# Optimization experiments

Measured on AMD Instinct MI355X. Metric: run time of the kernel, lower is better.

## Reference

```python
import jax, jax.numpy as jnp
import numpy as np

B, N_IN, NV, F = 1, 65536, 1, 64
N_OUT, K = 16384, 16
N_DIST, N_PHI, OUT = 4, 8, 256
DIST_MAX = 0.1  # grid_layers[level_out].min_dist stand-in


def setup_inputs() -> dict:
    key = jax.random.key(0)
    ks = jax.random.split(key, 6)
    x = jax.random.normal(ks[0], (B, N_IN, NV, F), dtype=jnp.float32)
    nh_idx = jax.random.randint(ks[1], (N_OUT, K), 0, N_IN)  # neighbor gather indices
    d_dists = jax.random.uniform(ks[2], (N_OUT, K), dtype=jnp.float32) * DIST_MAX
    d_phi = jax.random.uniform(ks[3], (N_OUT, K), dtype=jnp.float32) * (2 * np.pi) - np.pi
    dists = jnp.linspace(0.0, DIST_MAX, N_DIST, dtype=jnp.float32)          # anchor distances
    sigma = jnp.asarray(DIST_MAX / 2, dtype=jnp.float32)                     # n_sigma == 1 -> scalar
    phi = jnp.linspace(-np.pi, np.pi, N_PHI + 1, dtype=jnp.float32)[:-1]     # von Mises: phi_min = -pi
    kappa = jnp.asarray(1.0, dtype=jnp.float32)                              # kappa_init
    W_out = jax.random.normal(ks[4], (F * N_DIST * N_PHI, OUT), dtype=jnp.float32) / np.sqrt(F * N_DIST * N_PHI)
    return {"x": x, "d_dists": d_dists, "d_phi": d_phi, "dists": dists,
            "sigma": sigma, "kappa": kappa, "phi": phi, "W_out": W_out, "nh_idx": nh_idx}


def reference(x, d_dists, d_phi, dists, sigma, kappa, phi, W_out, nh_idx):
    # Gaussian distance kernel: exp(-0.5*((d - dist_k)/sigma)^2)  -> (N_OUT, K, N_DIST)
    w_d = jnp.exp(-0.5 * ((d_dists[..., None] - dists) / sigma) ** 2)
    # von Mises angular kernel: exp(kappa * cos(d_phi - phi_p))   -> (N_OUT, K, N_PHI)
    w_p = jnp.exp(kappa * jnp.cos(d_phi[..., None] - phi))
    # combined kernel weights, normalized over the K neighbors per anchor
    w = w_d[..., :, None] * w_p[..., None, :]                      # (N_OUT, K, N_DIST, N_PHI)
    w = w / (jnp.sum(w, axis=1, keepdims=True) + 1e-9)
    w = w.reshape(N_OUT, K, N_DIST * N_PHI)                        # (N_OUT, K, M)
    # gather neighbor features from the input grid
    x_nb = x[:, nh_idx]                                            # (B, N_OUT, K, NV, F)
    # weighted aggregation over neighbors -> enhanced channels
    agg = jnp.einsum('bnkvf,nkm->bnvmf', x_nb, w)                  # (B, N_OUT, NV, M, F)
    agg = agg.reshape(B, N_OUT, NV, N_DIST * N_PHI * F)            # model_dim_enhanced = 2048
    return agg @ W_out                                             # (B, N_OUT, NV, OUT)
```

## Files before the change

kernel.cpp:

```cpp
#include <hip/hip_runtime.h>
#include <hip/hip_bf16.h>

#define N_IN   65536
#define N_OUTP 16384
#define KNB    16
#define FDIM   64
#define M_DIM  32
#define KDIM   2048
#define OUT_D  256

typedef __bf16 bf16x8_t __attribute__((ext_vector_type(8)));
typedef float  f32x4_t  __attribute__((ext_vector_type(4)));


__device__ __forceinline__ unsigned pk2(float a, float b) {
  __bf16 b0 = (__bf16)a, b1 = (__bf16)b;
  return ((unsigned)__builtin_bit_cast(unsigned short, b1) << 16) |
          (unsigned)__builtin_bit_cast(unsigned short, b0);
}

__global__ __launch_bounds__(256) void pack_B_kernel(
    const float* __restrict__ W, uint4* __restrict__ Bws)
{
  int c    = blockIdx.x * 256 + threadIdx.x;
  int lane = c & 63;
  int nt   = (c >> 6) & 15;
  int kk   = c >> 10;
  int row0 = kk * 32 + (lane >> 4) * 8;
  int col  = nt * 16 + (lane & 15);
  union { unsigned short s[8]; uint4 v; } u;
#pragma unroll
  for (int j = 0; j < 8; ++j) {
    float f = W[(row0 + j) * OUT_D + col];
    __bf16 b = (__bf16)f;
    u.s[j] = __builtin_bit_cast(unsigned short, b);
  }
  Bws[c] = u.v;
}

#define WST 580
#define WKS 36
#define XST 1092
#define XKS 68

__global__ __launch_bounds__(256) void agg_kernel(
    const float* __restrict__ x,
    const float* __restrict__ d_dists,
    const float* __restrict__ d_phi,
    const float* __restrict__ dists,
    const float* __restrict__ sigma_p,
    const float* __restrict__ kappa_p,
    const float* __restrict__ phi,
    const int*   __restrict__ nh_idx,
    uint4*       __restrict__ Aws)
{
  __shared__ __align__(16) float wbuf[8 * WST];
  __shared__ __align__(16) float xbuf[8 * XST];

  const int t  = threadIdx.x;
  const int n0 = blockIdx.x * 8;
  const int T  = blockIdx.x >> 1;
  const int r0 = (blockIdx.x & 1) * 8;

  const int h = t & 1, gk = (t >> 1) & 15, gr8 = t >> 5;
  const int gidx = nh_idx[(n0 + gr8) * KNB + gk];
  const float4* xr = (const float4*)x + (size_t)gidx * 16 + h * 8;
  float4 xreg[8];
#pragma unroll
  for (int j = 0; j < 8; ++j) xreg[j] = xr[j];

  {
    const float sinv = 1.0f / sigma_p[0];
    const float kap  = kappa_p[0];
    float phiv[8], distv[4];
#pragma unroll
    for (int p = 0; p < 8; ++p) phiv[p] = phi[p];
#pragma unroll
    for (int d = 0; d < 4; ++d) distv[d] = dists[d];

    int rk = t >> 1, r8 = rk >> 4, k = rk & 15, rep = t & 1;
    int n = n0 + r8;
    float dd = d_dists[n * KNB + k];
    float dp = d_phi[n * KNB + k];
    float wp[8];
#pragma unroll
    for (int p = 0; p < 8; ++p) wp[p] = __expf(kap * __cosf(dp - phiv[p]));
#pragma unroll
    for (int dl = 0; dl < 2; ++dl) {
      int d = rep * 2 + dl;
      float td = (dd - distv[d]) * sinv;
      float wd = __expf(-0.5f * td * td);
      float* dst = wbuf + r8 * WST + k * WKS + d * 8;
      *(float4*)(dst)     = make_float4(wd * wp[0], wd * wp[1], wd * wp[2], wd * wp[3]);
      *(float4*)(dst + 4) = make_float4(wd * wp[4], wd * wp[5], wd * wp[6], wd * wp[7]);
    }
  }

  {
    float4* xd = (float4*)(xbuf + gr8 * XST + gk * XKS + h * 36);
#pragma unroll
    for (int j = 0; j < 8; ++j) xd[j] = xreg[j];
  }
  __syncthreads();

  {
    int r8 = t >> 5, m = t & 31;
    float wv[16];
    float s = 0.f;
#pragma unroll
    for (int k = 0; k < 16; ++k) {
      wv[k] = wbuf[r8 * WST + k * WKS + m];
      s += wv[k];
    }
    float wn = 1.0f / (s + 1e-9f);
#pragma unroll
    for (int k = 0; k < 16; ++k)
      wbuf[r8 * WST + k * WKS + m] = wv[k] * wn;
  }
  __syncthreads();

  {
    const int r8 = t & 7, fo = (t >> 3) & 7, mq = t >> 6;
    float acc[8][8];
#pragma unroll
    for (int mi = 0; mi < 8; ++mi)
#pragma unroll
      for (int fi = 0; fi < 8; ++fi) acc[mi][fi] = 0.f;

    const float* wp_ = wbuf + r8 * WST + mq * 8;
    const float* xp_ = xbuf + r8 * XST + ((fo < 4) ? fo * 8 : 36 + (fo - 4) * 8);

#pragma unroll 4
    for (int k = 0; k < 16; ++k) {
      float4 wa = *(const float4*)(wp_ + k * WKS);
      float4 wb = *(const float4*)(wp_ + k * WKS + 4);
      float4 xa = *(const float4*)(xp_ + k * XKS);
      float4 xb = *(const float4*)(xp_ + k * XKS + 4);
      float wv[8] = {wa.x, wa.y, wa.z, wa.w, wb.x, wb.y, wb.z, wb.w};
      float xv[8] = {xa.x, xa.y, xa.z, xa.w, xb.x, xb.y, xb.z, xb.w};
#pragma unroll
      for (int mi = 0; mi < 8; ++mi)
#pragma unroll
        for (int fi = 0; fi < 8; ++fi)
          acc[mi][fi] += wv[mi] * xv[fi];
    }

    uint4* base = Aws + (size_t)T * 4096 + (fo & 3) * 16 + r0 + r8
                      + (size_t)(fo >> 2) * 64;
#pragma unroll
    for (int mi = 0; mi < 8; ++mi) {
      int m = mq * 8 + mi;
      uint4 v;
      v.x = pk2(acc[mi][0], acc[mi][1]);
      v.y = pk2(acc[mi][2], acc[mi][3]);
      v.z = pk2(acc[mi][4], acc[mi][5]);
      v.w = pk2(acc[mi][6], acc[mi][7]);
      base[m * 128] = v;
    }
  }
}

__global__ __launch_bounds__(512) void gemm_kernel(
    const uint4* __restrict__ Astream,
    const uint4* __restrict__ Bws,
    float*       __restrict__ out)
{
  const int t    = threadIdx.x;
  const int lane = t & 63;
  const int w    = t >> 6;
  const int rb   = blockIdx.x;

  const uint4* pa = Astream + (size_t)(rb * 4 + (w & 1) * 2) * 4096 + lane;
  const uint4* pb = Bws + ((w >> 1) * 4) * 64 + lane;

  f32x4_t cacc[2][4];
#pragma unroll
  for (int mt = 0; mt < 2; ++mt)
#pragma unroll
    for (int i = 0; i < 4; ++i)
      cacc[mt][i] = (f32x4_t){0.f, 0.f, 0.f, 0.f};

  uint4 a[4][2], b[4][4];
#pragma unroll
  for (int s = 0; s < 4; ++s) {
    a[s][0] = pa[s * 64];
    a[s][1] = pa[4096 + s * 64];
#pragma unroll
    for (int i = 0; i < 4; ++i) b[s][i] = pb[s * 1024 + i * 64];
  }

#pragma unroll 4
  for (int kk = 0; kk < 64; ++kk) {
    const int s = kk & 3;
    bf16x8_t A0 = __builtin_bit_cast(bf16x8_t, a[s][0]);
    bf16x8_t A1 = __builtin_bit_cast(bf16x8_t, a[s][1]);
#pragma unroll
    for (int i = 0; i < 4; ++i) {
      bf16x8_t B = __builtin_bit_cast(bf16x8_t, b[s][i]);
      cacc[0][i] = __builtin_amdgcn_mfma_f32_16x16x32_bf16(A0, B, cacc[0][i], 0, 0, 0);
      cacc[1][i] = __builtin_amdgcn_mfma_f32_16x16x32_bf16(A1, B, cacc[1][i], 0, 0, 0);
    }
    if (kk < 60) {
      a[s][0] = pa[(kk + 4) * 64];
      a[s][1] = pa[4096 + (kk + 4) * 64];
#pragma unroll
      for (int i = 0; i < 4; ++i) b[s][i] = pb[(kk + 4) * 1024 + i * 64];
    }
  }

  const int rbase = rb * 64 + (w & 1) * 32 + (lane >> 4) * 4;
  const int cbase = (w >> 1) * 64 + (lane & 15);
#pragma unroll
  for (int mt = 0; mt < 2; ++mt)
#pragma unroll
    for (int i = 0; i < 4; ++i)
#pragma unroll
      for (int reg = 0; reg < 4; ++reg)
        out[(rbase + mt * 16 + reg) * OUT_D + cbase + i * 16] = cacc[mt][i][reg];
}

extern "C" void kernel_launch(void* const* d_in, const int* in_sizes, int n_in,
                              void* d_out, int out_size, void* d_ws, size_t ws_size,
                              hipStream_t stream) {
  const float* x      = (const float*)d_in[0];
  const float* dd     = (const float*)d_in[1];
  const float* dp     = (const float*)d_in[2];
  const float* dists  = (const float*)d_in[3];
  const float* sigma  = (const float*)d_in[4];
  const float* kappa  = (const float*)d_in[5];
  const float* phi    = (const float*)d_in[6];
  const float* W      = (const float*)d_in[7];
  const int*   nh     = (const int*)d_in[8];
  float*       out    = (float*)d_out;

  uint4* Bws = (uint4*)d_ws;
  uint4* Aws = (uint4*)((char*)d_ws + (1 << 20));

  pack_B_kernel<<<256, 256, 0, stream>>>(W, Bws);
  agg_kernel<<<N_OUTP / 8, 256, 0, stream>>>(
      x, dd, dp, dists, sigma, kappa, phi, nh, Aws);
  gemm_kernel<<<N_OUTP / 64, 512, 0, stream>>>(Aws, Bws, out);
}
```

Measured before the change: 64.95 us.

## Coalesce weight packing via LDS, pack FMAs in agg, retile GEMM to 4x4 MFMA per wave

pack_B now stages a 32-row slab of W in shared memory so global reads are coalesced, then transposes and converts it to bf16. The agg kernel's outer-product accumulation uses two-wide float vectors so the compiler can emit packed FMA instructions. The GEMM drops to 256 threads, and each wave now computes a 64x64 tile with 16 MFMAs per k-step, which increases A/B register reuse. Prefetch depth falls from 4 to 2, and there are fewer waves per block, so the GEMM may be less able to hide memory latency.

Result: faster. 62.75 us (-3.4%).

```diff
diff --git a/kernel.cpp b/kernel.cpp
--- a/kernel.cpp
+++ b/kernel.cpp
@@ -11,6 +11,7 @@
 
 typedef __bf16 bf16x8_t __attribute__((ext_vector_type(8)));
 typedef float  f32x4_t  __attribute__((ext_vector_type(4)));
+typedef float  f32x2_t  __attribute__((ext_vector_type(2)));
 
 
 __device__ __forceinline__ unsigned pk2(float a, float b) {
@@ -22,20 +23,33 @@
 __global__ __launch_bounds__(256) void pack_B_kernel(
     const float* __restrict__ W, uint4* __restrict__ Bws)
 {
-  int c    = blockIdx.x * 256 + threadIdx.x;
-  int lane = c & 63;
-  int nt   = (c >> 6) & 15;
-  int kk   = c >> 10;
-  int row0 = kk * 32 + (lane >> 4) * 8;
-  int col  = nt * 16 + (lane & 15);
-  union { unsigned short s[8]; uint4 v; } u;
-#pragma unroll
-  for (int j = 0; j < 8; ++j) {
-    float f = W[(row0 + j) * OUT_D + col];
-    __bf16 b = (__bf16)f;
-    u.s[j] = __builtin_bit_cast(unsigned short, b);
-  }
-  Bws[c] = u.v;
+  __shared__ float wlds[32 * 260];
+  const int kk = blockIdx.x;
+  const int t  = threadIdx.x;
+
+  const float4* Wb = (const float4*)(W + kk * 32 * OUT_D);
+#pragma unroll
+  for (int i = 0; i < 8; ++i) {
+    int idx = i * 256 + t;
+    int row = idx >> 6, c4 = idx & 63;
+    float4 v = Wb[idx];
+    *(float4*)(wlds + row * 260 + c4 * 4) = v;
+  }
+  __syncthreads();
+
+#pragma unroll
+  for (int j = 0; j < 4; ++j) {
+    int c  = j * 256 + t;
+    int l  = c & 63, nt = c >> 6;
+    int r0 = (l >> 4) * 8, col = nt * 16 + (l & 15);
+    union { unsigned short s[8]; uint4 v; } u;
+#pragma unroll
+    for (int jj = 0; jj < 8; ++jj) {
+      __bf16 b = (__bf16)wlds[(r0 + jj) * 260 + col];
+      u.s[jj] = __builtin_bit_cast(unsigned short, b);
+    }
+    Bws[(size_t)kk * 1024 + c] = u.v;
+  }
 }
 
 #define WST 580
@@ -121,28 +135,31 @@
 
   {
     const int r8 = t & 7, fo = (t >> 3) & 7, mq = t >> 6;
-    float acc[8][8];
+    f32x2_t acc[8][4];
 #pragma unroll
     for (int mi = 0; mi < 8; ++mi)
 #pragma unroll
-      for (int fi = 0; fi < 8; ++fi) acc[mi][fi] = 0.f;
+      for (int fj = 0; fj < 4; ++fj) acc[mi][fj] = (f32x2_t){0.f, 0.f};
 
     const float* wp_ = wbuf + r8 * WST + mq * 8;
     const float* xp_ = xbuf + r8 * XST + ((fo < 4) ? fo * 8 : 36 + (fo - 4) * 8);
 
-#pragma unroll 4
+#pragma unroll 8
     for (int k = 0; k < 16; ++k) {
       float4 wa = *(const float4*)(wp_ + k * WKS);
       float4 wb = *(const float4*)(wp_ + k * WKS + 4);
       float4 xa = *(const float4*)(xp_ + k * XKS);
       float4 xb = *(const float4*)(xp_ + k * XKS + 4);
       float wv[8] = {wa.x, wa.y, wa.z, wa.w, wb.x, wb.y, wb.z, wb.w};
-      float xv[8] = {xa.x, xa.y, xa.z, xa.w, xb.x, xb.y, xb.z, xb.w};
-#pragma unroll
-      for (int mi = 0; mi < 8; ++mi)
-#pragma unroll
-        for (int fi = 0; fi < 8; ++fi)
-          acc[mi][fi] += wv[mi] * xv[fi];
+      f32x2_t xv[4] = {(f32x2_t){xa.x, xa.y}, (f32x2_t){xa.z, xa.w},
+                       (f32x2_t){xb.x, xb.y}, (f32x2_t){xb.z, xb.w}};
+#pragma unroll
+      for (int mi = 0; mi < 8; ++mi) {
+        f32x2_t wm = (f32x2_t){wv[mi], wv[mi]};
+#pragma unroll
+        for (int fj = 0; fj < 4; ++fj)
+          acc[mi][fj] += wm * xv[fj];
+      }
     }
 
     uint4* base = Aws + (size_t)T * 4096 + (fo & 3) * 16 + r0 + r8
@@ -151,16 +168,16 @@
     for (int mi = 0; mi < 8; ++mi) {
       int m = mq * 8 + mi;
       uint4 v;
-      v.x = pk2(acc[mi][0], acc[mi][1]);
-      v.y = pk2(acc[mi][2], acc[mi][3]);
-      v.z = pk2(acc[mi][4], acc[mi][5]);
-      v.w = pk2(acc[mi][6], acc[mi][7]);
+      v.x = pk2(acc[mi][0][0], acc[mi][0][1]);
+      v.y = pk2(acc[mi][1][0], acc[mi][1][1]);
+      v.z = pk2(acc[mi][2][0], acc[mi][2][1]);
+      v.w = pk2(acc[mi][3][0], acc[mi][3][1]);
       base[m * 128] = v;
     }
   }
 }
 
-__global__ __launch_bounds__(512) void gemm_kernel(
+__global__ __launch_bounds__(256) void gemm_kernel(
     const uint4* __restrict__ Astream,
     const uint4* __restrict__ Bws,
     float*       __restrict__ out)
@@ -170,48 +187,52 @@
   const int w    = t >> 6;
   const int rb   = blockIdx.x;
 
-  const uint4* pa = Astream + (size_t)(rb * 4 + (w & 1) * 2) * 4096 + lane;
-  const uint4* pb = Bws + ((w >> 1) * 4) * 64 + lane;
-
-  f32x4_t cacc[2][4];
-#pragma unroll
-  for (int mt = 0; mt < 2; ++mt)
+  const uint4* pa = Astream + (size_t)(rb * 4) * 4096 + lane;
+  const uint4* pb = Bws + (w * 4) * 64 + lane;
+
+  f32x4_t cacc[4][4];
+#pragma unroll
+  for (int mt = 0; mt < 4; ++mt)
 #pragma unroll
     for (int i = 0; i < 4; ++i)
       cacc[mt][i] = (f32x4_t){0.f, 0.f, 0.f, 0.f};
 
-  uint4 a[4][2], b[4][4];
-#pragma unroll
-  for (int s = 0; s < 4; ++s) {
-    a[s][0] = pa[s * 64];
-    a[s][1] = pa[4096 + s * 64];
-#pragma unroll
-    for (int i = 0; i < 4; ++i) b[s][i] = pb[s * 1024 + i * 64];
+  uint4 a[2][4], b[2][4];
+#pragma unroll
+  for (int s = 0; s < 2; ++s) {
+#pragma unroll
+    for (int mt = 0; mt < 4; ++mt) a[s][mt] = pa[mt * 4096 + s * 64];
+#pragma unroll
+    for (int i = 0; i < 4; ++i)    b[s][i]  = pb[s * 1024 + i * 64];
   }
 
 #pragma unroll 4
   for (int kk = 0; kk < 64; ++kk) {
-    const int s = kk & 3;
-    bf16x8_t A0 = __builtin_bit_cast(bf16x8_t, a[s][0]);
-    bf16x8_t A1 = __builtin_bit_cast(bf16x8_t, a[s][1]);
-#pragma unroll
-    for (int i = 0; i < 4; ++i) {
-      bf16x8_t B = __builtin_bit_cast(bf16x8_t, b[s][i]);
-      cacc[0][i] = __builtin_amdgcn_mfma_f32_16x16x32_bf16(A0, B, cacc[0][i], 0, 0, 0);
-      cacc[1][i] = __builtin_amdgcn_mfma_f32_16x16x32_bf16(A1, B, cacc[1][i], 0, 0, 0);
-    }
-    if (kk < 60) {
-      a[s][0] = pa[(kk + 4) * 64];
-      a[s][1] = pa[4096 + (kk + 4) * 64];
-#pragma unroll
-      for (int i = 0; i < 4; ++i) b[s][i] = pb[(kk + 4) * 1024 + i * 64];
-    }
-  }
-
-  const int rbase = rb * 64 + (w & 1) * 32 + (lane >> 4) * 4;
-  const int cbase = (w >> 1) * 64 + (lane & 15);
-#pragma unroll
-  for (int mt = 0; mt < 2; ++mt)
+    const int s = kk & 1;
+    bf16x8_t B0 = __builtin_bit_cast(bf16x8_t, b[s][0]);
+    bf16x8_t B1 = __builtin_bit_cast(bf16x8_t, b[s][1]);
+    bf16x8_t B2 = __builtin_bit_cast(bf16x8_t, b[s][2]);
+    bf16x8_t B3 = __builtin_bit_cast(bf16x8_t, b[s][3]);
+#pragma unroll
+    for (int mt = 0; mt < 4; ++mt) {
+      bf16x8_t A = __builtin_bit_cast(bf16x8_t, a[s][mt]);
+      cacc[mt][0] = __builtin_amdgcn_mfma_f32_16x16x32_bf16(A, B0, cacc[mt][0], 0, 0, 0);
+      cacc[mt][1] = __builtin_amdgcn_mfma_f32_16x16x32_bf16(A, B1, cacc[mt][1], 0, 0, 0);
+      cacc[mt][2] = __builtin_amdgcn_mfma_f32_16x16x32_bf16(A, B2, cacc[mt][2], 0, 0, 0);
+      cacc[mt][3] = __builtin_amdgcn_mfma_f32_16x16x32_bf16(A, B3, cacc[mt][3], 0, 0, 0);
+    }
+    if (kk < 62) {
+#pragma unroll
+      for (int mt = 0; mt < 4; ++mt) a[s][mt] = pa[mt * 4096 + (kk + 2) * 64];
+#pragma unroll
+      for (int i = 0; i < 4; ++i)    b[s][i]  = pb[(kk + 2) * 1024 + i * 64];
+    }
+  }
+
+  const int rbase = rb * 64 + (lane >> 4) * 4;
+  const int cbase = w * 64 + (lane & 15);
+#pragma unroll
+  for (int mt = 0; mt < 4; ++mt)
 #pragma unroll
     for (int i = 0; i < 4; ++i)
 #pragma unroll
@@ -236,8 +257,8 @@
   uint4* Bws = (uint4*)d_ws;
   uint4* Aws = (uint4*)((char*)d_ws + (1 << 20));
 
-  pack_B_kernel<<<256, 256, 0, stream>>>(W, Bws);
+  pack_B_kernel<<<64, 256, 0, stream>>>(W, Bws);
   agg_kernel<<<N_OUTP / 8, 256, 0, stream>>>(
       x, dd, dp, dists, sigma, kappa, phi, nh, Aws);
-  gemm_kernel<<<N_OUTP / 64, 512, 0, stream>>>(Aws, Bws, out);
-}
+  gemm_kernel<<<N_OUTP / 64, 256, 0, stream>>>(Aws, Bws, out);
+}
```
